# Optimization experiments

Measured on AMD Instinct MI355X. Metric: run time of the kernel, lower is better.

Reference implementation:

```python
import jax, jax.numpy as jnp
import numpy as np
import math

D = 1024
H = 16
HD = D // H

def layernorm(x, g, b, eps=1e-5):
    mu = jnp.mean(x, axis=-1, keepdims=True)
    var = jnp.var(x, axis=-1, keepdims=True)
    return (x - mu) * jax.lax.rsqrt(var + eps) * g + b

def setup_inputs() -> dict:
    key = jax.random.key(0)
    ks = jax.random.split(key, 12)
    s = 0.02
    return {
        "x": jax.random.normal(ks[0], (2, 2048, D), jnp.float32),
        "Wk": jax.random.normal(ks[1], (D, D), jnp.float32) * s,
        "Wq": jax.random.normal(ks[2], (D, D), jnp.float32) * s,
        "Wv": jax.random.normal(ks[3], (D, D), jnp.float32) * s,
        "Wp": jax.random.normal(ks[4], (D, D), jnp.float32) * s,
        "bp": jnp.zeros((D,), jnp.float32),
        "g1": jnp.ones((D,), jnp.float32),
        "b1": jnp.zeros((D,), jnp.float32),
        "g2": jnp.ones((D,), jnp.float32),
        "b2": jnp.zeros((D,), jnp.float32),
        "W1": jax.random.normal(ks[5], (D, 4 * D), jnp.float32) * s,
        "bm1": jnp.zeros((4 * D,), jnp.float32),
        "W2": jax.random.normal(ks[6], (4 * D, D), jnp.float32) * s,
        "bm2": jnp.zeros((D,), jnp.float32),
    }

def reference(x, Wk, Wq, Wv, Wp, bp, g1, b1, g2, b2, W1, bm1, W2, bm2):
    B, S, _ = x.shape
    xn = layernorm(x, g1, b1)  # pre-LN; residual uses xn (faithful to source)
    # project and split heads -> [B, H, S, HD]
    def heads(y):
        return y.reshape(B, S, H, HD).transpose(0, 2, 1, 3)
    q = heads(xn @ Wq)
    k = heads(xn @ Wk)
    v = heads(xn @ Wv)
    scale = 1.0 / math.sqrt(HD)
    att = jnp.einsum('bhsd,bhtd->bhst', q, k) * scale  # [B,H,S,S]
    diag = jnp.eye(S, dtype=bool)
    att = jnp.where(diag, -jnp.inf, att)  # exclude self-attention on diagonal
    att = jax.nn.softmax(att, axis=-1)
    y = jnp.einsum('bhst,bhtd->bhsd', att, v)
    y = y.transpose(0, 2, 1, 3).reshape(B, S, D)
    y = y @ Wp + bp  # dropout is identity at inference
    h = xn + y
    hn = layernorm(h, g2, b2)
    mlp = jax.nn.gelu(hn @ W1 + bm1, approximate=False) @ W2 + bm2
    return h + mlp
```

## Files before the change

### kernel.cpp

```cpp
#include <hip/hip_runtime.h>
#include <hip/hip_bf16.h>
#include <math.h>

#define BATCH   2
#define SEQ     2048
#define D_MODEL 1024
#define NHEAD   16
#define HEADD   64
#define NROWS   (BATCH * SEQ)
#define D_FF    4096
#define TPARTS  4
#define TSPAN   (SEQ / TPARTS)

typedef __bf16 bf16_t;
typedef __bf16 bf16x2 __attribute__((ext_vector_type(2)));
typedef __bf16 bf16x4 __attribute__((ext_vector_type(4)));
typedef __bf16 bf16x8 __attribute__((ext_vector_type(8)));
typedef float  f32x4  __attribute__((ext_vector_type(4)));

#define QSCALE 0.18033688011112042f

__device__ __forceinline__ void gload_lds16(const void* g, void* l) {
    __builtin_amdgcn_global_load_lds(
        (const __attribute__((address_space(1))) unsigned int*)g,
        (__attribute__((address_space(3))) unsigned int*)l, 16, 0, 0);
}

__global__ __launch_bounds__(256) void transpose_to_bf16(
    const float* __restrict__ W, bf16_t* __restrict__ Wt, int K, int N)
{
    __shared__ float tile[32][33];
    int n0 = blockIdx.x * 32;
    int k0 = blockIdx.y * 32;
    int tx = threadIdx.x;
    int ty = threadIdx.y;
    #pragma unroll
    for (int i = 0; i < 32; i += 8)
        tile[ty + i][tx] = W[(size_t)(k0 + ty + i) * N + n0 + tx];
    __syncthreads();
    #pragma unroll
    for (int i = 0; i < 32; i += 8)
        Wt[(size_t)(n0 + ty + i) * K + k0 + tx] = (bf16_t)tile[tx][ty + i];
}

__global__ __launch_bounds__(256) void ln_kernel(
    const float* __restrict__ x, const float* __restrict__ g,
    const float* __restrict__ b, bf16_t* __restrict__ out)
{
    int row = blockIdx.x;
    int tid = threadIdx.x;
    const float* xr = x + (size_t)row * D_MODEL;
    f32x4 v = *(const f32x4*)(xr + tid * 4);
    float s  = v[0] + v[1] + v[2] + v[3];
    float s2 = v[0]*v[0] + v[1]*v[1] + v[2]*v[2] + v[3]*v[3];
    #pragma unroll
    for (int off = 32; off; off >>= 1) {
        s  += __shfl_down(s, off);
        s2 += __shfl_down(s2, off);
    }
    __shared__ float ps[4], ps2[4];
    int w = tid >> 6, lane = tid & 63;
    if (lane == 0) { ps[w] = s; ps2[w] = s2; }
    __syncthreads();
    float sum  = ps[0] + ps[1] + ps[2] + ps[3];
    float sum2 = ps2[0] + ps2[1] + ps2[2] + ps2[3];
    float mu  = sum * (1.0f / D_MODEL);
    float var = sum2 * (1.0f / D_MODEL) - mu * mu;
    float rs  = rsqrtf(var + 1e-5f);
    #pragma unroll
    for (int j = 0; j < 4; ++j) {
        int c = tid * 4 + j;
        out[(size_t)row * D_MODEL + c] = (bf16_t)((v[j] - mu) * rs * g[c] + b[c]);
    }
}

template<int EPI, int BN>
__global__ __launch_bounds__(256) void gemm128(
    const bf16_t* __restrict__ A, const bf16_t* __restrict__ Bt,
    const float* __restrict__ bias, const void* __restrict__ resid,
    void* __restrict__ out, int M, int N, int K)
{
    constexpr int JN = BN / 32;
    __shared__ bf16_t As[128 * 64];
    __shared__ bf16_t Bs[BN * 64];
    int tid = threadIdx.x;
    int m0 = blockIdx.x * 128;
    int n0 = blockIdx.y * BN;
    int w = tid >> 6, lane = tid & 63, quad = lane >> 4, l15 = lane & 15;
    int wm = (w & 1) * 64, wn = (w >> 1) * (BN / 2);
    int srow = tid >> 3;
    int sxor = (((tid & 7) ^ (srow & 7)) << 3);

    const bf16_t* Ap = A  + (size_t)(m0 + srow) * K + sxor;
    const bf16_t* Bp = Bt + (size_t)(n0 + srow) * K + sxor;
    bf16_t* AsW = As + w * 512;
    bf16_t* BsW = Bs + w * 512;

    int rxs = l15 & 7;

    f32x4 acc[4][JN] = {};

    for (int k0 = 0; k0 < K; k0 += 64) {
        __syncthreads();
        #pragma unroll
        for (int p = 0; p < 4; ++p)
            gload_lds16(Ap + (size_t)p * 32 * K + k0, AsW + p * 2048);
        #pragma unroll
        for (int p = 0; p < BN / 32; ++p)
            gload_lds16(Bp + (size_t)p * 32 * K + k0, BsW + p * 2048);
        __syncthreads();
        #pragma unroll
        for (int kk = 0; kk < 2; ++kk) {
            bf16x8 af[4], bfr[JN];
            #pragma unroll
            for (int i = 0; i < 4; ++i)
                af[i] = *(const bf16x8*)&As[(wm + i * 16 + l15) * 64
                                            + ((((kk << 2) | quad) ^ rxs) << 3)];
            #pragma unroll
            for (int j = 0; j < JN; ++j)
                bfr[j] = *(const bf16x8*)&Bs[(wn + j * 16 + l15) * 64
                                            + ((((kk << 2) | quad) ^ rxs) << 3)];
            #pragma unroll
            for (int i = 0; i < 4; ++i)
                #pragma unroll
                for (int j = 0; j < JN; ++j)
                    acc[i][j] = __builtin_amdgcn_mfma_f32_16x16x32_bf16(af[i], bfr[j], acc[i][j], 0, 0, 0);
        }
    }

    #pragma unroll
    for (int i = 0; i < 4; ++i)
    #pragma unroll
    for (int j = 0; j < JN; ++j) {
        int col  = n0 + wn + j * 16 + l15;
        int row0 = m0 + wm + i * 16 + quad * 4;
        if (EPI == 6) {
            int region = (n0 + wn + j * 16) >> 10;
            if (region < 2) {
                #pragma unroll
                for (int r = 0; r < 4; ++r) {
                    int row = row0 + r;
                    float v = acc[i][j][r];
                    if (region == 0) v *= QSCALE;
                    int b = row >> 11, s = row & 2047, hh = (col & 1023) >> 6, d = col & 63;
                    bf16_t* dst = (bf16_t*)out + (size_t)region * 4194304;
                    dst[(((size_t)(b * NHEAD + hh)) * SEQ + s) * HEADD + d] = (bf16_t)v;
                }
            } else {
                int dg = col - 2048, hh = dg >> 6, d = dg & 63;
                int b = row0 >> 11, s0 = row0 & 2047;
                bf16x4 pv;
                #pragma unroll
                for (int r = 0; r < 4; ++r) pv[r] = (bf16_t)acc[i][j][r];
                *(bf16x4*)((bf16_t*)out + 8388608
                           + (((size_t)(b * NHEAD + hh)) * HEADD + d) * SEQ + s0) = pv;
            }
        } else {
            float bv = bias[col];
            #pragma unroll
            for (int r = 0; r < 4; ++r) {
                int row = row0 + r;
                float vacc = acc[i][j][r] + bv;
                if (EPI == 1) {
                    float res = (float)((const bf16_t*)resid)[(size_t)row * N + col];
                    ((float*)out)[(size_t)row * N + col] = vacc + res;
                } else if (EPI == 2) {
                    float gl = 0.5f * vacc * (1.0f + erff(vacc * 0.70710678118654752f));
                    ((bf16_t*)out)[(size_t)row * N + col] = (bf16_t)gl;
                } else {
                    float res = ((const float*)resid)[(size_t)row * N + col];
                    ((float*)out)[(size_t)row * N + col] = vacc + res;
                }
            }
        }
    }
}

__global__ __launch_bounds__(256, 4) void attn_kernel(
    const bf16_t* __restrict__ q, const bf16_t* __restrict__ k,
    const bf16_t* __restrict__ vt, bf16_t* __restrict__ po,
    float* __restrict__ plsum)
{
    int gid = blockIdx.x;
    int xcd = gid & 7;
    int loc = gid >> 3;
    int bh  = xcd * 4 + (loc >> 6);
    int rest = loc & 63;
    int qt   = rest >> 2;
    int part = rest & 3;
    int tb0 = part * TSPAN, tend = tb0 + TSPAN;
    int b = bh >> 4, h = bh & 15;
    int tid = threadIdx.x, w = tid >> 6, lane = tid & 63;
    int quad = lane >> 4, l15 = lane & 15;
    int qbase = qt * 128 + w * 32;
    const bf16_t* qh = q  + (size_t)bh * SEQ * HEADD;
    const bf16_t* kh = k  + (size_t)bh * SEQ * HEADD;
    const bf16_t* vh = vt + (size_t)bh * HEADD * SEQ;

    bf16x8 qa[2][2];
    #pragma unroll
    for (int m = 0; m < 2; ++m)
        #pragma unroll
        for (int hf = 0; hf < 2; ++hf)
            qa[m][hf] = *(const bf16x8*)(qh + (size_t)(qbase + m * 16 + l15) * HEADD + hf * 32 + quad * 8);

    bf16x8 ones;
    #pragma unroll
    for (int j = 0; j < 8; ++j) ones[j] = (bf16_t)1.0f;

    __shared__ alignas(16) bf16_t Ks[32 * 72];
    __shared__ alignas(16) bf16_t Vs[64 * 40];
    __shared__ alignas(16) bf16_t Pl[4][32][40];

    int ksrow = tid >> 3, kscol = (tid & 7) * 8;
    int vsrow = tid >> 2, vscol = (tid & 3) * 8;
    const bf16_t* kg = kh + (size_t)ksrow * HEADD + kscol;
    const bf16_t* vg = vh + (size_t)vsrow * SEQ + vscol;

    f32x4 o[2][4] = {};
    f32x4 ls[2] = {};

    for (int t0 = tb0; t0 < tend; t0 += 32) {
        bf16x8 kreg = *(const bf16x8*)(kg + (size_t)t0 * HEADD);
        bf16x8 vreg = *(const bf16x8*)(vg + t0);
        __syncthreads();
        *(bf16x8*)&Ks[ksrow * 72 + kscol] = kreg;
        *(bf16x8*)&Vs[vsrow * 40 + vscol] = vreg;
        __syncthreads();

        bf16x8 kb[2][2], vf[4];
        #pragma unroll
        for (int jt = 0; jt < 2; ++jt)
            #pragma unroll
            for (int hf = 0; hf < 2; ++hf)
                kb[jt][hf] = *(const bf16x8*)&Ks[(2 * l15 + jt) * 72 + hf * 32 + quad * 8];
        #pragma unroll
        for (int dn = 0; dn < 4; ++dn)
            vf[dn] = *(const bf16x8*)&Vs[(dn * 16 + l15) * 40 + quad * 8];

        #pragma unroll
        for (int m = 0; m < 2; ++m) {
            f32x4 sc[2];
            #pragma unroll
            for (int jt = 0; jt < 2; ++jt) {
                f32x4 z = {};
                z = __builtin_amdgcn_mfma_f32_16x16x32_bf16(qa[m][0], kb[jt][0], z, 0, 0, 0);
                z = __builtin_amdgcn_mfma_f32_16x16x32_bf16(qa[m][1], kb[jt][1], z, 0, 0, 0);
                sc[jt] = z;
            }
            int qm = qbase + m * 16;
            bool dg = (t0 < qm + 16) && (t0 + 32 > qm);
            #pragma unroll
            for (int r = 0; r < 4; ++r) {
                int qrow = qm + quad * 4 + r;
                float p0 = __builtin_amdgcn_exp2f(sc[0][r]);
                float p1 = __builtin_amdgcn_exp2f(sc[1][r]);
                if (dg) {
                    int tg = t0 + 2 * l15;
                    if (tg == qrow)     p0 = 0.0f;
                    if (tg + 1 == qrow) p1 = 0.0f;
                }
                bf16x2 pp = { (bf16_t)p0, (bf16_t)p1 };
                *(bf16x2*)&Pl[w][m * 16 + quad * 4 + r][2 * l15] = pp;
            }
        }
        #pragma unroll
        for (int m = 0; m < 2; ++m) {
            bf16x8 pf = *(const bf16x8*)&Pl[w][m * 16 + l15][quad * 8];
            ls[m] = __builtin_amdgcn_mfma_f32_16x16x32_bf16(pf, ones, ls[m], 0, 0, 0);
            #pragma unroll
            for (int dn = 0; dn < 4; ++dn)
                o[m][dn] = __builtin_amdgcn_mfma_f32_16x16x32_bf16(pf, vf[dn], o[m][dn], 0, 0, 0);
        }
    }

    #pragma unroll
    for (int m = 0; m < 2; ++m)
        #pragma unroll
        for (int dn = 0; dn < 4; ++dn)
            #pragma unroll
            for (int r = 0; r < 4; ++r) {
                int qrow = qbase + m * 16 + quad * 4 + r;
                po[(((size_t)part * NROWS) + b * SEQ + qrow) * D_MODEL
                   + h * HEADD + dn * 16 + l15] = (bf16_t)o[m][dn][r];
            }
    if (l15 == 0) {
        #pragma unroll
        for (int m = 0; m < 2; ++m)
            #pragma unroll
            for (int r = 0; r < 4; ++r) {
                int qrow = qbase + m * 16 + quad * 4 + r;
                plsum[((size_t)part * 32 + bh) * SEQ + qrow] = ls[m][r];
            }
    }
}

__global__ __launch_bounds__(256) void attn_merge(
    const bf16_t* __restrict__ po, const float* __restrict__ plsum,
    bf16_t* __restrict__ y)
{
    int row = blockIdx.x;
    int tid = threadIdx.x;
    int c = tid * 4;
    int b = row >> 11, s = row & 2047;
    int bh = b * NHEAD + (c >> 6);
    float l = 0.0f;
    f32x4 ov = {};
    #pragma unroll
    for (int p = 0; p < TPARTS; ++p) {
        l += plsum[((size_t)p * 32 + bh) * SEQ + s];
        bf16x4 t = *(const bf16x4*)&po[((size_t)p * NROWS + row) * D_MODEL + c];
        #pragma unroll
        for (int j = 0; j < 4; ++j) ov[j] += (float)t[j];
    }
    float rl = 1.0f / l;
    bf16x4 out;
    #pragma unroll
    for (int j = 0; j < 4; ++j) out[j] = (bf16_t)(ov[j] * rl);
    *(bf16x4*)&y[(size_t)row * D_MODEL + c] = out;
}

extern "C" void kernel_launch(void* const* d_in, const int* in_sizes, int n_in,
                              void* d_out, int out_size, void* d_ws, size_t ws_size,
                              hipStream_t stream)
{
    const float* x   = (const float*)d_in[0];
    const float* Wk  = (const float*)d_in[1];
    const float* Wq  = (const float*)d_in[2];
    const float* Wv  = (const float*)d_in[3];
    const float* Wp  = (const float*)d_in[4];
    const float* bp  = (const float*)d_in[5];
    const float* g1  = (const float*)d_in[6];
    const float* b1  = (const float*)d_in[7];
    const float* g2  = (const float*)d_in[8];
    const float* b2  = (const float*)d_in[9];
    const float* W1  = (const float*)d_in[10];
    const float* bm1 = (const float*)d_in[11];
    const float* W2  = (const float*)d_in[12];
    const float* bm2 = (const float*)d_in[13];

    char* ws = (char*)d_ws;
    const size_t MB = 1024 * 1024;
    bf16_t* Wqkvt = (bf16_t*)(ws + 0 * MB);
    bf16_t* Wpt = (bf16_t*)(ws + 6 * MB);
    bf16_t* W1t = (bf16_t*)(ws + 8 * MB);
    bf16_t* W2t = (bf16_t*)(ws + 16 * MB);
    bf16_t* xn  = (bf16_t*)(ws + 24 * MB);
    bf16_t* qkv = (bf16_t*)(ws + 32 * MB);
    bf16_t* qb  = (bf16_t*)(ws + 32 * MB);
    bf16_t* kb  = (bf16_t*)(ws + 40 * MB);
    bf16_t* vtb = (bf16_t*)(ws + 48 * MB);
    bf16_t* yb  = (bf16_t*)(ws + 56 * MB);
    float*  hbuf= (float*) (ws + 64 * MB);
    bf16_t* po  = (bf16_t*)(ws + 64 * MB);
    float*  pls = (float*) (ws + 96 * MB);
    bf16_t* hn  = (bf16_t*)(ws + 24 * MB);
    bf16_t* act = (bf16_t*)(ws + 32 * MB);

    dim3 tb(32, 8);
    transpose_to_bf16<<<dim3(32, 32), tb, 0, stream>>>(Wq, Wqkvt,               1024, 1024);
    transpose_to_bf16<<<dim3(32, 32), tb, 0, stream>>>(Wk, Wqkvt + 1024 * 1024, 1024, 1024);
    transpose_to_bf16<<<dim3(32, 32), tb, 0, stream>>>(Wv, Wqkvt + 2048 * 1024, 1024, 1024);
    transpose_to_bf16<<<dim3(32, 32), tb, 0, stream>>>(Wp, Wpt, 1024, 1024);
    transpose_to_bf16<<<dim3(128, 32), tb, 0, stream>>>(W1, W1t, 1024, 4096);
    transpose_to_bf16<<<dim3(32, 128), tb, 0, stream>>>(W2, W2t, 4096, 1024);

    ln_kernel<<<NROWS, 256, 0, stream>>>(x, g1, b1, xn);

    gemm128<6, 128><<<dim3(32, 24), 256, 0, stream>>>(xn, Wqkvt, nullptr, nullptr, qkv, NROWS, 3072, D_MODEL);

    attn_kernel<<<2048, 256, 0, stream>>>(qb, kb, vtb, po, pls);
    attn_merge<<<NROWS, 256, 0, stream>>>(po, pls, yb);

    gemm128<1, 64><<<dim3(32, 16), 256, 0, stream>>>(yb, Wpt, bp, xn, hbuf, NROWS, D_MODEL, D_MODEL);

    ln_kernel<<<NROWS, 256, 0, stream>>>(hbuf, g2, b2, hn);

    gemm128<2, 128><<<dim3(32, 32), 256, 0, stream>>>(hn, W1t, bm1, nullptr, act, NROWS, D_FF, D_MODEL);
    gemm128<3, 64><<<dim3(32, 16), 256, 0, stream>>>(act, W2t, bm2, hbuf, d_out, NROWS, D_MODEL, D_FF);
}
```

Before: 384.4 us.

## Double-buffer LDS in GEMM K-loop and use tanh-form GELU

Adds two LDS buffers to the GEMM so the next K tile's global-to-LDS loads are issued before computing on the current tile. Explicit vmcnt waits and barriers replace the two syncthreads per iteration. The goal is to overlap memory latency with MFMA work, at the cost of doubled LDS use and possibly lower occupancy. It also replaces the erf-based GELU with an exp2/rcp tanh-style approximation, which cuts epilogue cost but changes numerics slightly.

```diff
diff --git a/kernel.cpp b/kernel.cpp
--- a/kernel.cpp
+++ b/kernel.cpp
@@ -81,8 +81,8 @@
     void* __restrict__ out, int M, int N, int K)
 {
     constexpr int JN = BN / 32;
-    __shared__ bf16_t As[128 * 64];
-    __shared__ bf16_t Bs[BN * 64];
+    __shared__ bf16_t As[2][128 * 64];
+    __shared__ bf16_t Bs[2][BN * 64];
     int tid = threadIdx.x;
     int m0 = blockIdx.x * 128;
     int n0 = blockIdx.y * BN;
@@ -93,32 +93,45 @@
 
     const bf16_t* Ap = A  + (size_t)(m0 + srow) * K + sxor;
     const bf16_t* Bp = Bt + (size_t)(n0 + srow) * K + sxor;
-    bf16_t* AsW = As + w * 512;
-    bf16_t* BsW = Bs + w * 512;
 
     int rxs = l15 & 7;
 
-    f32x4 acc[4][JN] = {};
-
-    for (int k0 = 0; k0 < K; k0 += 64) {
-        __syncthreads();
+    auto stage = [&](int buf, int k0) {
+        bf16_t* AsW = &As[buf][w * 512];
+        bf16_t* BsW = &Bs[buf][w * 512];
         #pragma unroll
         for (int p = 0; p < 4; ++p)
             gload_lds16(Ap + (size_t)p * 32 * K + k0, AsW + p * 2048);
         #pragma unroll
-        for (int p = 0; p < BN / 32; ++p)
+        for (int p = 0; p < JN; ++p)
             gload_lds16(Bp + (size_t)p * 32 * K + k0, BsW + p * 2048);
-        __syncthreads();
+    };
+
+    f32x4 acc[4][JN] = {};
+
+    int nt = K >> 6;
+    stage(0, 0);
+    for (int t = 0; t < nt; ++t) {
+        int cur = t & 1;
+        if (t + 1 < nt) {
+            stage(cur ^ 1, (t + 1) << 6);
+            if constexpr (BN == 128) asm volatile("s_waitcnt vmcnt(8)" ::: "memory");
+            else                     asm volatile("s_waitcnt vmcnt(6)" ::: "memory");
+        } else {
+            asm volatile("s_waitcnt vmcnt(0)" ::: "memory");
+        }
+        __builtin_amdgcn_s_barrier();
+        __builtin_amdgcn_sched_barrier(0);
         #pragma unroll
         for (int kk = 0; kk < 2; ++kk) {
             bf16x8 af[4], bfr[JN];
             #pragma unroll
             for (int i = 0; i < 4; ++i)
-                af[i] = *(const bf16x8*)&As[(wm + i * 16 + l15) * 64
+                af[i] = *(const bf16x8*)&As[cur][(wm + i * 16 + l15) * 64
                                             + ((((kk << 2) | quad) ^ rxs) << 3)];
             #pragma unroll
             for (int j = 0; j < JN; ++j)
-                bfr[j] = *(const bf16x8*)&Bs[(wn + j * 16 + l15) * 64
+                bfr[j] = *(const bf16x8*)&Bs[cur][(wn + j * 16 + l15) * 64
                                             + ((((kk << 2) | quad) ^ rxs) << 3)];
             #pragma unroll
             for (int i = 0; i < 4; ++i)
@@ -126,6 +139,10 @@
                 for (int j = 0; j < JN; ++j)
                     acc[i][j] = __builtin_amdgcn_mfma_f32_16x16x32_bf16(af[i], bfr[j], acc[i][j], 0, 0, 0);
         }
+        __builtin_amdgcn_sched_barrier(0);
+        asm volatile("s_waitcnt lgkmcnt(0)" ::: "memory");
+        __builtin_amdgcn_s_barrier();
+        __builtin_amdgcn_sched_barrier(0);
     }
 
     #pragma unroll
@@ -165,8 +182,11 @@
                     float res = (float)((const bf16_t*)resid)[(size_t)row * N + col];
                     ((float*)out)[(size_t)row * N + col] = vacc + res;
                 } else if (EPI == 2) {
-                    float gl = 0.5f * vacc * (1.0f + erff(vacc * 0.70710678118654752f));
-                    ((bf16_t*)out)[(size_t)row * N + col] = (bf16_t)gl;
+                    float u = vacc;
+                    float y = u * (0.7978845608028654f + 0.03567740814f * u * u);
+                    float e = __builtin_amdgcn_exp2f(2.8853900817779268f * y);
+                    float r8 = __builtin_amdgcn_rcpf(e + 1.0f);
+                    ((bf16_t*)out)[(size_t)row * N + col] = (bf16_t)(u - u * r8);
                 } else {
                     float res = ((const float*)resid)[(size_t)row * N + col];
                     ((float*)out)[(size_t)row * N + col] = vacc + res;
```

After: 354.6 us. 1.08x faster.
